# Kernel tuning notes

Hardware: AMD Instinct MI355X
Metric: run time of the kernel (lower is better)

Reference implementation:

```python
import jax, jax.numpy as jnp
import numpy as np

EPS = 1e-15
PROJ_EPS = 1e-5
N_NODES = 100000

def _norm(x):
    return jnp.maximum(jnp.sqrt(jnp.sum(x * x, axis=-1, keepdims=True)), EPS)

def _tanh(x):
    return jnp.tanh(jnp.clip(x, -15.0, 15.0))

def _atanh(x):
    return jnp.arctanh(jnp.clip(x, -1.0 + 1e-7, 1.0 - 1e-7))

def log_map_zero(y):
    n = _norm(y)
    return (_atanh(n) / n) * y

def exp_map_zero(v):
    n = _norm(v)
    return (_tanh(n) / n) * v

def hyperbolic_projection(x):
    # clip norm to 1 - PROJ_EPS (stay inside the Poincare ball)
    n = _norm(x)
    scale = jnp.minimum(jnp.float32(1.0), (1.0 - PROJ_EPS) / n)
    return x * scale

def mobius_addition(x, y):
    x2 = jnp.sum(x * x, axis=-1, keepdims=True)
    y2 = jnp.sum(y * y, axis=-1, keepdims=True)
    xy = jnp.sum(x * y, axis=-1, keepdims=True)
    num = (1.0 + 2.0 * xy + y2) * x + (1.0 - x2) * y
    den = 1.0 + 2.0 * xy + x2 * y2
    return num / jnp.maximum(den, EPS)

def setup_inputs() -> dict:
    key = jax.random.key(0)
    k0, k1, k2, k3, k4, k5 = jax.random.split(key, 6)
    N, E, D_IN, D_OUT = N_NODES, 640000, 128, 128
    # entity embeddings: points inside the Poincare ball
    x = jax.random.normal(k0, (N, D_IN), dtype=jnp.float32) * 0.01
    x = hyperbolic_projection(x)
    # xavier-uniform weight
    a = np.sqrt(6.0 / (D_IN + D_OUT)).astype(np.float32)
    W = jax.random.uniform(k1, (D_IN, D_OUT), minval=-a, maxval=a, dtype=jnp.float32)
    bias = jax.random.normal(k2, (1, D_OUT), dtype=jnp.float32) * 0.01
    adj_row = jax.random.randint(k3, (E,), 0, N, dtype=jnp.int32)
    adj_col = jax.random.randint(k4, (E,), 0, N, dtype=jnp.int32)
    adj_val = jax.random.uniform(k5, (E,), dtype=jnp.float32) * 0.125
    return {"ents_embed_input": x, "W_ent": W, "bias_vec": bias,
            "adj_val": adj_val, "adj_row": adj_row, "adj_col": adj_col}

def reference(ents_embed_input, W_ent, bias_vec, adj_val, adj_row, adj_col):
    # log map to tangent space at origin, then dense linear map
    tangent = log_map_zero(ents_embed_input)                 # [N, D_in]
    mapped = tangent @ W_ent                                 # [N, D_out]
    # sparse adjacency aggregation: out[i] = sum_e val[e] * mapped[col[e]], row[e] == i
    msgs = adj_val[:, None] * mapped[adj_col]                # [E, D_out]
    agg = jax.ops.segment_sum(msgs, adj_row, num_segments=N_NODES)
    h = hyperbolic_projection(exp_map_zero(agg))
    # mobius bias addition
    b = hyperbolic_projection(exp_map_zero(bias_vec))
    out = hyperbolic_projection(mobius_addition(h, b))
    return out
```

## Files before the change

kernel.cpp:

```cpp
#include <hip/hip_runtime.h>
#include <hip/hip_bf16.h>

#define D 128
#define FEPS 1e-15f
#define PROJ_EPS 1e-5f

typedef __attribute__((ext_vector_type(8))) short short8v;
typedef __attribute__((ext_vector_type(4))) float f32x4;

__device__ __forceinline__ unsigned pack_bf16x2(float lo, float hi) {
    __hip_bfloat16 h0 = __float2bfloat16(lo);
    __hip_bfloat16 h1 = __float2bfloat16(hi);
    unsigned u0 = *reinterpret_cast<unsigned short*>(&h0);
    unsigned u1 = *reinterpret_cast<unsigned short*>(&h1);
    return u0 | (u1 << 16);
}

__device__ __forceinline__ float bf_lo(unsigned u) { return __uint_as_float(u << 16); }
__device__ __forceinline__ float bf_hi(unsigned u) { return __uint_as_float(u & 0xffff0000u); }

__device__ __forceinline__ float fast_tanh_clamped(float n) {
    float nc = fminf(n, 15.f);
    float e2 = __expf(2.f * nc);
    return 1.f - __fdividef(2.f, e2 + 1.f);
}

__global__ __launch_bounds__(512) void k_hist8(const int* __restrict__ rowi,
                                               int* __restrict__ cnt8,
                                               int E, int Nn, int Eper) {
    int e = blockIdx.x * 512 + threadIdx.x;
    if (e < E) {
        int g = e / Eper;
        atomicAdd(&cnt8[(size_t)g * Nn + rowi[e]], 1);
    }
}

__global__ __launch_bounds__(256) void k_scan1(const int* __restrict__ cnt,
                                               int* __restrict__ ex,
                                               int* __restrict__ bsum, int Ntot) {
    __shared__ int ts[256];
    int t = threadIdx.x, b = blockIdx.x;
    int base = b * 1024 + t * 4;
    int v0 = (base + 0 < Ntot) ? cnt[base + 0] : 0;
    int v1 = (base + 1 < Ntot) ? cnt[base + 1] : 0;
    int v2 = (base + 2 < Ntot) ? cnt[base + 2] : 0;
    int v3 = (base + 3 < Ntot) ? cnt[base + 3] : 0;
    int s = v0 + v1 + v2 + v3;
    ts[t] = s;
    __syncthreads();
    for (int off = 1; off < 256; off <<= 1) {
        int add = (t >= off) ? ts[t - off] : 0;
        __syncthreads();
        ts[t] += add;
        __syncthreads();
    }
    int excl = ts[t] - s;
    if (t == 255) bsum[b] = ts[t];
    if (base + 0 < Ntot) ex[base + 0] = excl;
    if (base + 1 < Ntot) ex[base + 1] = excl + v0;
    if (base + 2 < Ntot) ex[base + 2] = excl + v0 + v1;
    if (base + 3 < Ntot) ex[base + 3] = excl + v0 + v1 + v2;
}

__global__ __launch_bounds__(1024) void k_scan2(const int* __restrict__ bsum,
                                                int* __restrict__ bsumx, int nb) {
    __shared__ int ts[1024];
    int t = threadIdx.x;
    int v = (t < nb) ? bsum[t] : 0;
    ts[t] = v;
    __syncthreads();
    for (int off = 1; off < 1024; off <<= 1) {
        int add = (t >= off) ? ts[t - off] : 0;
        __syncthreads();
        ts[t] += add;
        __syncthreads();
    }
    bsumx[t] = ts[t] - v;
}

__global__ __launch_bounds__(256) void k_scan3(int* __restrict__ base8,
                                               const int* __restrict__ bsumx,
                                               int* __restrict__ cursor8,
                                               int Ntot, int E) {
    int i = blockIdx.x * 256 + threadIdx.x;
    if (i < Ntot) {
        int v = base8[i] + bsumx[i >> 10];
        base8[i] = v;
        cursor8[i] = v;
    }
    if (i == 0) base8[Ntot] = E;
}

__global__ __launch_bounds__(512) void k_gemm_scatter(
    const float* __restrict__ x, const float* __restrict__ W,
    __hip_bfloat16* __restrict__ mapped, int Nn, int NT, int GBg,
    const int* __restrict__ rowi, const int* __restrict__ coli,
    const float* __restrict__ val, int* __restrict__ cursor8,
    int2* __restrict__ sedge, int E)
{
    __shared__ uint4 lsW4[2048];
    __shared__ uint4 lsC4[2048];

    const int tid = threadIdx.x;

    if (blockIdx.x >= GBg) {
        const int j = blockIdx.x - GBg;
        const int g = j & 7;
        const int ib = j >> 3;
        const int Echunk = (E + 127) >> 7;
        const int chunk = g * 16 + ib;
        int e0 = chunk * Echunk;
        int e1 = min(e0 + Echunk, E);
        int* cur = cursor8 + (size_t)g * Nn;
        for (int e = e0 + tid; e < e1; e += 512) {
            int r = rowi[e];
            int cv = coli[e];
            float vv = val[e];
            int p = atomicAdd(&cur[r], 1);
            sedge[p] = make_int2(cv, __float_as_int(vv));
        }
        return;
    }

    const int w = tid >> 6, l = tid & 63;
    const int q = l & 15, khi = l >> 4;

#pragma unroll
    for (int it = 0; it < 4; ++it) {
        int i = it * 512 + tid;
        int col = i & 127, kg = i >> 7;
        unsigned p0 = pack_bf16x2(W[(kg * 8 + 0) * D + col], W[(kg * 8 + 1) * D + col]);
        unsigned p1 = pack_bf16x2(W[(kg * 8 + 2) * D + col], W[(kg * 8 + 3) * D + col]);
        unsigned p2 = pack_bf16x2(W[(kg * 8 + 4) * D + col], W[(kg * 8 + 5) * D + col]);
        unsigned p3 = pack_bf16x2(W[(kg * 8 + 6) * D + col], W[(kg * 8 + 7) * D + col]);
        lsW4[col * 16 + (kg ^ (col & 15))] = make_uint4(p0, p1, p2, p3);
    }
    __syncthreads();

    const short8v* lsB = (const short8v*)lsW4;
    unsigned* lsc = (unsigned*)lsC4;
    const int cbase = w * 1024;

#pragma unroll 1
    for (int tt = blockIdx.x; tt < NT; tt += GBg) {
        const int rowbase = tt * 128;
        const int row = rowbase + w * 16 + q;
        const bool rv = row < Nn;
        const float* xr = x + (size_t)row * D;
        float4 xa[8];
        float nn = 0.f;
#pragma unroll
        for (int ks = 0; ks < 4; ++ks) {
            float4 p0 = make_float4(0.f, 0.f, 0.f, 0.f), p1 = p0;
            if (rv) {
                p0 = *reinterpret_cast<const float4*>(xr + ks * 32 + khi * 8);
                p1 = *reinterpret_cast<const float4*>(xr + ks * 32 + khi * 8 + 4);
            }
            xa[2 * ks] = p0; xa[2 * ks + 1] = p1;
            nn += p0.x * p0.x + p0.y * p0.y + p0.z * p0.z + p0.w * p0.w
                + p1.x * p1.x + p1.y * p1.y + p1.z * p1.z + p1.w * p1.w;
        }
        nn += __shfl_xor(nn, 16, 64);
        nn += __shfl_xor(nn, 32, 64);
        float n = fmaxf(sqrtf(nn), FEPS);
        float c = fminf(n, 1.f - 1e-7f);
        float s = __fdividef(0.5f * __logf(__fdividef(1.f + c, 1.f - c)), n);

        union { unsigned u[4]; short8v v; } af[4];
#pragma unroll
        for (int ks = 0; ks < 4; ++ks) {
            float4 p0 = xa[2 * ks], p1 = xa[2 * ks + 1];
            af[ks].u[0] = pack_bf16x2(s * p0.x, s * p0.y);
            af[ks].u[1] = pack_bf16x2(s * p0.z, s * p0.w);
            af[ks].u[2] = pack_bf16x2(s * p1.x, s * p1.y);
            af[ks].u[3] = pack_bf16x2(s * p1.z, s * p1.w);
        }

        f32x4 acc[8];
#pragma unroll
        for (int t = 0; t < 8; ++t) acc[t] = (f32x4){0.f, 0.f, 0.f, 0.f};

#pragma unroll
        for (int ks = 0; ks < 4; ++ks) {
#pragma unroll
            for (int t = 0; t < 8; ++t) {
                short8v b = lsB[(t * 16 + q) * 16 + ((ks * 4 + khi) ^ q)];
                acc[t] = __builtin_amdgcn_mfma_f32_16x16x32_bf16(af[ks].v, b, acc[t], 0, 0, 0);
            }
        }

#pragma unroll
        for (int t = 0; t < 8; ++t) {
#pragma unroll
            for (int r = 0; r < 4; ++r) {
                float self = acc[t][r];
                float other = __shfl_xor(self, 1, 64);
                unsigned pw = (q & 1) ? pack_bf16x2(other, self) : pack_bf16x2(self, other);
                int rl = khi * 4 + r;
                int cp = t * 8 + (q >> 1);
                lsc[cbase + rl * 64 + (cp ^ (khi << 3))] = pw;
            }
        }
#pragma unroll
        for (int i4 = 0; i4 < 4; ++i4) {
            int rl = i4 * 4 + (l >> 4);
            int ro = rowbase + w * 16 + rl;
            int cp4 = (l & 15) * 4;
            uint4 vv = lsC4[(cbase + rl * 64 + (cp4 ^ (i4 << 3))) >> 2];
            if (ro < Nn)
                *reinterpret_cast<uint4*>(mapped + (size_t)ro * D + (l & 15) * 8) = vv;
        }
    }
}

__device__ __forceinline__ void accum8(float* acc, uint4 u, float v) {
    acc[0] += v * bf_lo(u.x); acc[1] += v * bf_hi(u.x);
    acc[2] += v * bf_lo(u.y); acc[3] += v * bf_hi(u.y);
    acc[4] += v * bf_lo(u.z); acc[5] += v * bf_hi(u.z);
    acc[6] += v * bf_lo(u.w); acc[7] += v * bf_hi(u.w);
}

__global__ __launch_bounds__(256) void k_aggfin(
    const uint4* __restrict__ mapped4, const int2* __restrict__ sedge,
    const int* __restrict__ base8, const float* __restrict__ bias,
    float* __restrict__ out, int Nn)
{
    const int tid = threadIdx.x;
    const int w = tid >> 6, l = tid & 63;
    const int g = l >> 4, q = l & 15;
    const int row = blockIdx.x * 16 + w * 4 + g;

    float4 rb0 = *reinterpret_cast<const float4*>(bias + q * 8);
    float4 rb1 = *reinterpret_cast<const float4*>(bias + q * 8 + 4);
    float bn2 = rb0.x * rb0.x + rb0.y * rb0.y + rb0.z * rb0.z + rb0.w * rb0.w
              + rb1.x * rb1.x + rb1.y * rb1.y + rb1.z * rb1.z + rb1.w * rb1.w;
#pragma unroll
    for (int o = 8; o > 0; o >>= 1) bn2 += __shfl_xor(bn2, o, 64);
    float bn = fmaxf(sqrtf(bn2), FEPS);
    float bt = fast_tanh_clamped(bn);
    float bs = __fdividef(bt, bn);
    float ben2 = bs * bs * bn2;
    float bpn = fmaxf(sqrtf(ben2), FEPS);
    float bps = fminf(1.f, __fdividef(1.f - PROJ_EPS, bpn));
    float bsc = bs * bps;
    float y2 = bps * bps * ben2;
    float bj[8] = { rb0.x * bsc, rb0.y * bsc, rb0.z * bsc, rb0.w * bsc,
                    rb1.x * bsc, rb1.y * bsc, rb1.z * bsc, rb1.w * bsc };

    if (row >= Nn) return;

    int hdr = base8[(size_t)(q & 7) * Nn + row + (q >> 3)];
    const int gl = l & 48;
    int b[8], en_[8];
#pragma unroll
    for (int s2 = 0; s2 < 8; ++s2) {
        b[s2]   = __shfl(hdr, gl + s2, 64);
        en_[s2] = __shfl(hdr, gl + 8 + s2, 64);
    }

    float acc[8] = {0.f, 0.f, 0.f, 0.f, 0.f, 0.f, 0.f, 0.f};
    while (true) {
        int2 d[4]; bool h[4];
#pragma unroll
        for (int s = 0; s < 4; ++s) {
            int p = -1;
            if (b[s] < en_[s])            { p = b[s]; b[s] += 1; }
            else if (b[s + 4] < en_[s + 4]) { p = b[s + 4]; b[s + 4] += 1; }
            h[s] = (p >= 0);
            if (h[s]) d[s] = sedge[p];
        }
        uint4 u[4];
#pragma unroll
        for (int s = 0; s < 4; ++s)
            if (h[s]) u[s] = mapped4[(size_t)d[s].x * 16 + q];
#pragma unroll
        for (int s = 0; s < 4; ++s)
            if (h[s]) accum8(acc, u[s], __int_as_float(d[s].y));
        bool any = false;
#pragma unroll
        for (int s = 0; s < 8; ++s) any = any || (b[s] < en_[s]);
        if (!any) break;
    }

    float n2 = 0.f, ab = 0.f;
#pragma unroll
    for (int j = 0; j < 8; ++j) { n2 += acc[j] * acc[j]; ab += acc[j] * bj[j]; }
#pragma unroll
    for (int o = 8; o > 0; o >>= 1) {
        n2 += __shfl_xor(n2, o, 64);
        ab += __shfl_xor(ab, o, 64);
    }

    float n = fmaxf(sqrtf(n2), FEPS);
    float t = fast_tanh_clamped(n);
    float s = __fdividef(t, n);
    float en2 = s * s * n2;
    float pn = fmaxf(sqrtf(en2), FEPS);
    float ps = fminf(1.f, __fdividef(1.f - PROJ_EPS, pn));
    float hs = s * ps;
    float x2 = ps * ps * en2;

    float xy = hs * ab;
    float cA = 1.f + 2.f * xy + y2;
    float cB = 1.f - x2;
    float den = fmaxf(1.f + 2.f * xy + x2 * y2, FEPS);
    float inv = __fdividef(1.f, den);
    float zn2 = inv * inv * (cA * cA * x2 + 2.f * cA * cB * xy + cB * cB * y2);
    float zn = fmaxf(sqrtf(zn2), FEPS);
    float zs = fminf(1.f, __fdividef(1.f - PROJ_EPS, zn));
    float f = inv * zs;
    float chs = cA * hs * f, cBf = cB * f;

    float4 o0 = make_float4(chs * acc[0] + cBf * bj[0], chs * acc[1] + cBf * bj[1],
                            chs * acc[2] + cBf * bj[2], chs * acc[3] + cBf * bj[3]);
    float4 o1 = make_float4(chs * acc[4] + cBf * bj[4], chs * acc[5] + cBf * bj[5],
                            chs * acc[6] + cBf * bj[6], chs * acc[7] + cBf * bj[7]);
    *reinterpret_cast<float4*>(out + (size_t)row * D + q * 8) = o0;
    *reinterpret_cast<float4*>(out + (size_t)row * D + q * 8 + 4) = o1;
}

extern "C" void kernel_launch(void* const* d_in, const int* in_sizes, int n_in,
                              void* d_out, int out_size, void* d_ws, size_t ws_size,
                              hipStream_t stream) {
    const float* x    = (const float*)d_in[0];
    const float* W    = (const float*)d_in[1];
    const float* bias = (const float*)d_in[2];
    const float* val  = (const float*)d_in[3];
    const int*   rowi = (const int*)d_in[4];
    const int*   coli = (const int*)d_in[5];
    const int N = in_sizes[0] / D;
    const int E = in_sizes[3];
    const int N8 = 8 * N;

    char* ws = (char*)d_ws;
    size_t off = 0;
    int* cnt8 = (int*)(ws + off);      off += (size_t)N8 * 4;
    int* base8 = (int*)(ws + off);     off += ((size_t)N8 + 1) * 4;
    off = (off + 63) & ~(size_t)63;
    int* bsum = (int*)(ws + off);      off += 1024 * 4;
    int* bsumx = (int*)(ws + off);     off += 1024 * 4;
    int* cursor8 = (int*)(ws + off);   off += (size_t)N8 * 4;
    off = (off + 63) & ~(size_t)63;
    int2* sedge = (int2*)(ws + off);   off += (size_t)E * 8;
    __hip_bfloat16* mapped = (__hip_bfloat16*)(ws + off);
    float* out = (float*)d_out;

    const int Echunk = (E + 127) >> 7;
    const int Eper = 16 * Echunk;

    hipMemsetAsync(cnt8, 0, (size_t)N8 * sizeof(int), stream);
    k_hist8<<<(E + 511) / 512, 512, 0, stream>>>(rowi, cnt8, E, N, Eper);

    int nb = (N8 + 1023) / 1024;
    k_scan1<<<nb, 256, 0, stream>>>(cnt8, base8, bsum, N8);
    k_scan2<<<1, 1024, 0, stream>>>(bsum, bsumx, nb);
    k_scan3<<<(N8 + 255) / 256, 256, 0, stream>>>(base8, bsumx, cursor8, N8, E);

    const int NT  = (N + 127) / 128;
    const int GBg = 384;
    k_gemm_scatter<<<GBg + 128, 512, 0, stream>>>(x, W, mapped, N, NT, GBg,
                                                  rowi, coli, val, cursor8, sedge, E);

    k_aggfin<<<(N + 15) / 16, 256, 0, stream>>>((const uint4*)mapped,
                                                (const int2*)sedge, base8,
                                                bias, out, N);
}
```

Baseline: 149.7 us.

## Replace per-row CSR sort with 120-row bucket binning and LDS atomic aggregation

Drops the 8-way per-row histogram and three-pass scan. Edges are instead binned into buckets of 120 destination rows, so only about 834 bucket counters need a single-block scan. The scatter blocks now do a block-local counting sort in shared memory before writing coalesced records. Aggregation runs one block per bucket and accumulates into a shared-memory float tile with LDS atomics. This cuts scan and global-atomic overhead but adds shared-memory atomic contention, wider 16-byte edge records, and makes the float summation order nondeterministic.

```diff
diff --git a/kernel.cpp b/kernel.cpp
--- a/kernel.cpp
+++ b/kernel.cpp
@@ -4,6 +4,9 @@
 #define D 128
 #define FEPS 1e-15f
 #define PROJ_EPS 1e-5f
+#define BROWS 120
+#define BSTRIDE 132
+#define SC 3072
 
 typedef __attribute__((ext_vector_type(8))) short short8v;
 typedef __attribute__((ext_vector_type(4))) float f32x4;
@@ -25,48 +28,18 @@
     return 1.f - __fdividef(2.f, e2 + 1.f);
 }
 
-__global__ __launch_bounds__(512) void k_hist8(const int* __restrict__ rowi,
-                                               int* __restrict__ cnt8,
-                                               int E, int Nn, int Eper) {
+__global__ __launch_bounds__(512) void k_bhist(const int* __restrict__ rowi,
+                                               int* __restrict__ bcntP, int E) {
     int e = blockIdx.x * 512 + threadIdx.x;
-    if (e < E) {
-        int g = e / Eper;
-        atomicAdd(&cnt8[(size_t)g * Nn + rowi[e]], 1);
-    }
-}
-
-__global__ __launch_bounds__(256) void k_scan1(const int* __restrict__ cnt,
-                                               int* __restrict__ ex,
-                                               int* __restrict__ bsum, int Ntot) {
-    __shared__ int ts[256];
-    int t = threadIdx.x, b = blockIdx.x;
-    int base = b * 1024 + t * 4;
-    int v0 = (base + 0 < Ntot) ? cnt[base + 0] : 0;
-    int v1 = (base + 1 < Ntot) ? cnt[base + 1] : 0;
-    int v2 = (base + 2 < Ntot) ? cnt[base + 2] : 0;
-    int v3 = (base + 3 < Ntot) ? cnt[base + 3] : 0;
-    int s = v0 + v1 + v2 + v3;
-    ts[t] = s;
-    __syncthreads();
-    for (int off = 1; off < 256; off <<= 1) {
-        int add = (t >= off) ? ts[t - off] : 0;
-        __syncthreads();
-        ts[t] += add;
-        __syncthreads();
-    }
-    int excl = ts[t] - s;
-    if (t == 255) bsum[b] = ts[t];
-    if (base + 0 < Ntot) ex[base + 0] = excl;
-    if (base + 1 < Ntot) ex[base + 1] = excl + v0;
-    if (base + 2 < Ntot) ex[base + 2] = excl + v0 + v1;
-    if (base + 3 < Ntot) ex[base + 3] = excl + v0 + v1 + v2;
-}
-
-__global__ __launch_bounds__(1024) void k_scan2(const int* __restrict__ bsum,
-                                                int* __restrict__ bsumx, int nb) {
+    if (e < E) atomicAdd(&bcntP[(rowi[e] / BROWS) * 16], 1);
+}
+
+__global__ __launch_bounds__(1024) void k_bscan(const int* __restrict__ bcntP,
+                                                int* __restrict__ bbase,
+                                                int* __restrict__ bcursor, int NB) {
     __shared__ int ts[1024];
     int t = threadIdx.x;
-    int v = (t < nb) ? bsum[t] : 0;
+    int v = (t < NB) ? bcntP[t * 16] : 0;
     ts[t] = v;
     __syncthreads();
     for (int off = 1; off < 1024; off <<= 1) {
@@ -75,53 +48,99 @@
         ts[t] += add;
         __syncthreads();
     }
-    bsumx[t] = ts[t] - v;
-}
-
-__global__ __launch_bounds__(256) void k_scan3(int* __restrict__ base8,
-                                               const int* __restrict__ bsumx,
-                                               int* __restrict__ cursor8,
-                                               int Ntot, int E) {
-    int i = blockIdx.x * 256 + threadIdx.x;
-    if (i < Ntot) {
-        int v = base8[i] + bsumx[i >> 10];
-        base8[i] = v;
-        cursor8[i] = v;
-    }
-    if (i == 0) base8[Ntot] = E;
-}
-
-__global__ __launch_bounds__(512) void k_gemm_scatter(
+    int ex = ts[t] - v;
+    if (t < NB) { bbase[t] = ex; bcursor[t] = ex; }
+    if (t == NB - 1) bbase[NB] = ex + v;
+}
+
+__global__ __launch_bounds__(512) void k_gemm_bin(
     const float* __restrict__ x, const float* __restrict__ W,
-    __hip_bfloat16* __restrict__ mapped, int Nn, int NT, int GBg,
+    __hip_bfloat16* __restrict__ mapped, int Nn, int NT, int GBg, int SBb,
     const int* __restrict__ rowi, const int* __restrict__ coli,
-    const float* __restrict__ val, int* __restrict__ cursor8,
-    int2* __restrict__ sedge, int E)
+    const float* __restrict__ val, int* __restrict__ bcursor,
+    int4* __restrict__ brec, int E, int NB)
 {
-    __shared__ uint4 lsW4[2048];
-    __shared__ uint4 lsC4[2048];
+    __shared__ uint4 ls4[4096];
 
     const int tid = threadIdx.x;
 
     if (blockIdx.x >= GBg) {
+        char* base = (char*)ls4;
+        int4* srec  = (int4*)base;
+        int* lhist  = (int*)(base + 49152);
+        int* lstart = (int*)(base + 53248);
+        int* gb     = (int*)(base + 57344);
+        int* scr    = (int*)(base + 60704);
+
         const int j = blockIdx.x - GBg;
-        const int g = j & 7;
-        const int ib = j >> 3;
-        const int Echunk = (E + 127) >> 7;
-        const int chunk = g * 16 + ib;
-        int e0 = chunk * Echunk;
-        int e1 = min(e0 + Echunk, E);
-        int* cur = cursor8 + (size_t)g * Nn;
-        for (int e = e0 + tid; e < e1; e += 512) {
-            int r = rowi[e];
-            int cv = coli[e];
-            float vv = val[e];
-            int p = atomicAdd(&cur[r], 1);
-            sedge[p] = make_int2(cv, __float_as_int(vv));
+        const int NC = (E + SC - 1) / SC;
+        for (int ci = j; ci < NC; ci += SBb) {
+            const int e0 = ci * SC;
+            const int cnt = min(SC, E - e0);
+
+            for (int b = tid; b < 1024; b += 512) lhist[b] = 0;
+            __syncthreads();
+
+            int rr[6], cc[6], vi[6], bb[6];
+#pragma unroll
+            for (int k = 0; k < 6; ++k) {
+                int idx = k * 512 + tid;
+                if (idx < cnt) {
+                    int e = e0 + idx;
+                    rr[k] = rowi[e]; cc[k] = coli[e];
+                    vi[k] = __float_as_int(val[e]);
+                    bb[k] = rr[k] / BROWS;
+                    atomicAdd(&lhist[bb[k]], 1);
+                }
+            }
+            __syncthreads();
+
+            {
+                int a0 = lhist[2 * tid], a1 = lhist[2 * tid + 1];
+                int ps = a0 + a1;
+                scr[tid] = ps;
+                __syncthreads();
+                for (int off = 1; off < 512; off <<= 1) {
+                    int add = (tid >= off) ? scr[tid - off] : 0;
+                    __syncthreads();
+                    scr[tid] += add;
+                    __syncthreads();
+                }
+                int ex = scr[tid] - ps;
+                lstart[2 * tid] = ex;
+                lstart[2 * tid + 1] = ex + a0;
+            }
+            __syncthreads();
+            for (int b = tid; b < 840; b += 512) scr[b] = lstart[b];
+            __syncthreads();
+
+#pragma unroll
+            for (int k = 0; k < 6; ++k) {
+                int idx = k * 512 + tid;
+                if (idx < cnt) {
+                    int slot = atomicAdd(&scr[bb[k]], 1);
+                    srec[slot] = make_int4(rr[k], cc[k], vi[k], bb[k]);
+                }
+            }
+            __syncthreads();
+
+            for (int b = tid; b < NB; b += 512) {
+                int cb = lhist[b];
+                gb[b] = cb ? atomicAdd(&bcursor[b], cb) : 0;
+            }
+            __syncthreads();
+
+            for (int i = tid; i < cnt; i += 512) {
+                int4 rec = srec[i];
+                brec[gb[rec.w] + (i - lstart[rec.w])] = rec;
+            }
+            __syncthreads();
         }
         return;
     }
 
+    uint4* lsW4 = ls4;
+    uint4* lsC4 = ls4 + 2048;
     const int w = tid >> 6, l = tid & 63;
     const int q = l & 15, khi = l >> 4;
 
@@ -179,7 +198,6 @@
         f32x4 acc[8];
 #pragma unroll
         for (int t = 0; t < 8; ++t) acc[t] = (f32x4){0.f, 0.f, 0.f, 0.f};
-
 #pragma unroll
         for (int ks = 0; ks < 4; ++ks) {
 #pragma unroll
@@ -213,25 +231,23 @@
     }
 }
 
-__device__ __forceinline__ void accum8(float* acc, uint4 u, float v) {
-    acc[0] += v * bf_lo(u.x); acc[1] += v * bf_hi(u.x);
-    acc[2] += v * bf_lo(u.y); acc[3] += v * bf_hi(u.y);
-    acc[4] += v * bf_lo(u.z); acc[5] += v * bf_hi(u.z);
-    acc[6] += v * bf_lo(u.w); acc[7] += v * bf_hi(u.w);
-}
-
-__global__ __launch_bounds__(256) void k_aggfin(
-    const uint4* __restrict__ mapped4, const int2* __restrict__ sedge,
-    const int* __restrict__ base8, const float* __restrict__ bias,
+__global__ __launch_bounds__(512) void k_aggfin_lds(
+    const uint2* __restrict__ mapped2, const int4* __restrict__ brec,
+    const int* __restrict__ bbase, const float* __restrict__ bias,
     float* __restrict__ out, int Nn)
 {
+    __shared__ float facc[BROWS][BSTRIDE];
+
     const int tid = threadIdx.x;
-    const int w = tid >> 6, l = tid & 63;
-    const int g = l >> 4, q = l & 15;
-    const int row = blockIdx.x * 16 + w * 4 + g;
-
-    float4 rb0 = *reinterpret_cast<const float4*>(bias + q * 8);
-    float4 rb1 = *reinterpret_cast<const float4*>(bias + q * 8 + 4);
+    const int l = tid & 63;
+    const int q = l & 15;
+
+    float4* fz = (float4*)&facc[0][0];
+    for (int i = tid; i < (BROWS * BSTRIDE) / 4; i += 512)
+        fz[i] = make_float4(0.f, 0.f, 0.f, 0.f);
+
+    float4 rb0 = *reinterpret_cast<const float4*>(bias + 4 * q);
+    float4 rb1 = *reinterpret_cast<const float4*>(bias + 64 + 4 * q);
     float bn2 = rb0.x * rb0.x + rb0.y * rb0.y + rb0.z * rb0.z + rb0.w * rb0.w
               + rb1.x * rb1.x + rb1.y * rb1.y + rb1.z * rb1.z + rb1.w * rb1.w;
 #pragma unroll
@@ -247,76 +263,75 @@
     float bj[8] = { rb0.x * bsc, rb0.y * bsc, rb0.z * bsc, rb0.w * bsc,
                     rb1.x * bsc, rb1.y * bsc, rb1.z * bsc, rb1.w * bsc };
 
-    if (row >= Nn) return;
-
-    int hdr = base8[(size_t)(q & 7) * Nn + row + (q >> 3)];
-    const int gl = l & 48;
-    int b[8], en_[8];
-#pragma unroll
-    for (int s2 = 0; s2 < 8; ++s2) {
-        b[s2]   = __shfl(hdr, gl + s2, 64);
-        en_[s2] = __shfl(hdr, gl + 8 + s2, 64);
-    }
-
-    float acc[8] = {0.f, 0.f, 0.f, 0.f, 0.f, 0.f, 0.f, 0.f};
-    while (true) {
-        int2 d[4]; bool h[4];
-#pragma unroll
-        for (int s = 0; s < 4; ++s) {
-            int p = -1;
-            if (b[s] < en_[s])            { p = b[s]; b[s] += 1; }
-            else if (b[s + 4] < en_[s + 4]) { p = b[s + 4]; b[s + 4] += 1; }
-            h[s] = (p >= 0);
-            if (h[s]) d[s] = sedge[p];
-        }
-        uint4 u[4];
-#pragma unroll
-        for (int s = 0; s < 4; ++s)
-            if (h[s]) u[s] = mapped4[(size_t)d[s].x * 16 + q];
-#pragma unroll
-        for (int s = 0; s < 4; ++s)
-            if (h[s]) accum8(acc, u[s], __int_as_float(d[s].y));
-        bool any = false;
-#pragma unroll
-        for (int s = 0; s < 8; ++s) any = any || (b[s] < en_[s]);
-        if (!any) break;
-    }
-
-    float n2 = 0.f, ab = 0.f;
-#pragma unroll
-    for (int j = 0; j < 8; ++j) { n2 += acc[j] * acc[j]; ab += acc[j] * bj[j]; }
-#pragma unroll
-    for (int o = 8; o > 0; o >>= 1) {
-        n2 += __shfl_xor(n2, o, 64);
-        ab += __shfl_xor(ab, o, 64);
-    }
-
-    float n = fmaxf(sqrtf(n2), FEPS);
-    float t = fast_tanh_clamped(n);
-    float s = __fdividef(t, n);
-    float en2 = s * s * n2;
-    float pn = fmaxf(sqrtf(en2), FEPS);
-    float ps = fminf(1.f, __fdividef(1.f - PROJ_EPS, pn));
-    float hs = s * ps;
-    float x2 = ps * ps * en2;
-
-    float xy = hs * ab;
-    float cA = 1.f + 2.f * xy + y2;
-    float cB = 1.f - x2;
-    float den = fmaxf(1.f + 2.f * xy + x2 * y2, FEPS);
-    float inv = __fdividef(1.f, den);
-    float zn2 = inv * inv * (cA * cA * x2 + 2.f * cA * cB * xy + cB * cB * y2);
-    float zn = fmaxf(sqrtf(zn2), FEPS);
-    float zs = fminf(1.f, __fdividef(1.f - PROJ_EPS, zn));
-    float f = inv * zs;
-    float chs = cA * hs * f, cBf = cB * f;
-
-    float4 o0 = make_float4(chs * acc[0] + cBf * bj[0], chs * acc[1] + cBf * bj[1],
-                            chs * acc[2] + cBf * bj[2], chs * acc[3] + cBf * bj[3]);
-    float4 o1 = make_float4(chs * acc[4] + cBf * bj[4], chs * acc[5] + cBf * bj[5],
-                            chs * acc[6] + cBf * bj[6], chs * acc[7] + cBf * bj[7]);
-    *reinterpret_cast<float4*>(out + (size_t)row * D + q * 8) = o0;
-    *reinterpret_cast<float4*>(out + (size_t)row * D + q * 8 + 4) = o1;
+    __syncthreads();
+
+    const int bkt = blockIdx.x;
+    const int beg = bbase[bkt], end = bbase[bkt + 1];
+    const int grp = tid >> 4;
+
+    for (int e = beg + grp; e < end; e += 32) {
+        int4 rec = brec[e];
+        float v = __int_as_float(rec.z);
+        int rl = rec.x - bkt * BROWS;
+        uint2 m0 = mapped2[(size_t)rec.y * 32 + q];
+        uint2 m1 = mapped2[(size_t)rec.y * 32 + 16 + q];
+        atomicAdd(&facc[rl][4 * q + 0], v * bf_lo(m0.x));
+        atomicAdd(&facc[rl][4 * q + 1], v * bf_hi(m0.x));
+        atomicAdd(&facc[rl][4 * q + 2], v * bf_lo(m0.y));
+        atomicAdd(&facc[rl][4 * q + 3], v * bf_hi(m0.y));
+        atomicAdd(&facc[rl][64 + 4 * q + 0], v * bf_lo(m1.x));
+        atomicAdd(&facc[rl][64 + 4 * q + 1], v * bf_hi(m1.x));
+        atomicAdd(&facc[rl][64 + 4 * q + 2], v * bf_lo(m1.y));
+        atomicAdd(&facc[rl][64 + 4 * q + 3], v * bf_hi(m1.y));
+    }
+    __syncthreads();
+
+    const int w = tid >> 6, g = l >> 4;
+#pragma unroll
+    for (int r4 = 0; r4 < 4; ++r4) {
+        int rl = w * 16 + r4 * 4 + g;
+        int row = bkt * BROWS + rl;
+        if (rl >= BROWS || row >= Nn) continue;
+        float4 f0 = *(float4*)&facc[rl][4 * q];
+        float4 f1 = *(float4*)&facc[rl][64 + 4 * q];
+        float a[8] = { f0.x, f0.y, f0.z, f0.w, f1.x, f1.y, f1.z, f1.w };
+
+        float n2 = 0.f, ab = 0.f;
+#pragma unroll
+        for (int jj = 0; jj < 8; ++jj) { n2 += a[jj] * a[jj]; ab += a[jj] * bj[jj]; }
+#pragma unroll
+        for (int o = 8; o > 0; o >>= 1) {
+            n2 += __shfl_xor(n2, o, 64);
+            ab += __shfl_xor(ab, o, 64);
+        }
+
+        float n = fmaxf(sqrtf(n2), FEPS);
+        float t = fast_tanh_clamped(n);
+        float s = __fdividef(t, n);
+        float en2 = s * s * n2;
+        float pn = fmaxf(sqrtf(en2), FEPS);
+        float ps = fminf(1.f, __fdividef(1.f - PROJ_EPS, pn));
+        float hs = s * ps;
+        float x2 = ps * ps * en2;
+
+        float xy = hs * ab;
+        float cA = 1.f + 2.f * xy + y2;
+        float cB = 1.f - x2;
+        float den = fmaxf(1.f + 2.f * xy + x2 * y2, FEPS);
+        float inv = __fdividef(1.f, den);
+        float zn2 = inv * inv * (cA * cA * x2 + 2.f * cA * cB * xy + cB * cB * y2);
+        float zn = fmaxf(sqrtf(zn2), FEPS);
+        float zs = fminf(1.f, __fdividef(1.f - PROJ_EPS, zn));
+        float f = inv * zs;
+        float chs = cA * hs * f, cBf = cB * f;
+
+        float4 o0 = make_float4(chs * a[0] + cBf * bj[0], chs * a[1] + cBf * bj[1],
+                                chs * a[2] + cBf * bj[2], chs * a[3] + cBf * bj[3]);
+        float4 o1 = make_float4(chs * a[4] + cBf * bj[4], chs * a[5] + cBf * bj[5],
+                                chs * a[6] + cBf * bj[6], chs * a[7] + cBf * bj[7]);
+        *reinterpret_cast<float4*>(out + (size_t)row * D + 4 * q) = o0;
+        *reinterpret_cast<float4*>(out + (size_t)row * D + 64 + 4 * q) = o1;
+    }
 }
 
 extern "C" void kernel_launch(void* const* d_in, const int* in_sizes, int n_in,
@@ -330,38 +345,28 @@
     const int*   coli = (const int*)d_in[5];
     const int N = in_sizes[0] / D;
     const int E = in_sizes[3];
-    const int N8 = 8 * N;
+    const int NB = (N + BROWS - 1) / BROWS;
 
     char* ws = (char*)d_ws;
     size_t off = 0;
-    int* cnt8 = (int*)(ws + off);      off += (size_t)N8 * 4;
-    int* base8 = (int*)(ws + off);     off += ((size_t)N8 + 1) * 4;
-    off = (off + 63) & ~(size_t)63;
-    int* bsum = (int*)(ws + off);      off += 1024 * 4;
-    int* bsumx = (int*)(ws + off);     off += 1024 * 4;
-    int* cursor8 = (int*)(ws + off);   off += (size_t)N8 * 4;
-    off = (off + 63) & ~(size_t)63;
-    int2* sedge = (int2*)(ws + off);   off += (size_t)E * 8;
+    int* bcntP  = (int*)(ws + off);  off += (size_t)NB * 64;
+    int* bbase  = (int*)(ws + off);  off += ((size_t)NB + 1) * 4;
+    int* bcursor= (int*)(ws + off);  off += (size_t)NB * 4;
+    off = (off + 15) & ~(size_t)15;
+    int4* brec  = (int4*)(ws + off); off += (size_t)E * 16;
     __hip_bfloat16* mapped = (__hip_bfloat16*)(ws + off);
     float* out = (float*)d_out;
 
-    const int Echunk = (E + 127) >> 7;
-    const int Eper = 16 * Echunk;
-
-    hipMemsetAsync(cnt8, 0, (size_t)N8 * sizeof(int), stream);
-    k_hist8<<<(E + 511) / 512, 512, 0, stream>>>(rowi, cnt8, E, N, Eper);
-
-    int nb = (N8 + 1023) / 1024;
-    k_scan1<<<nb, 256, 0, stream>>>(cnt8, base8, bsum, N8);
-    k_scan2<<<1, 1024, 0, stream>>>(bsum, bsumx, nb);
-    k_scan3<<<(N8 + 255) / 256, 256, 0, stream>>>(base8, bsumx, cursor8, N8, E);
+    hipMemsetAsync(bcntP, 0, (size_t)NB * 64, stream);
+    k_bhist<<<(E + 511) / 512, 512, 0, stream>>>(rowi, bcntP, E);
+    k_bscan<<<1, 1024, 0, stream>>>(bcntP, bbase, bcursor, NB);
 
     const int NT  = (N + 127) / 128;
     const int GBg = 384;
-    k_gemm_scatter<<<GBg + 128, 512, 0, stream>>>(x, W, mapped, N, NT, GBg,
-                                                  rowi, coli, val, cursor8, sedge, E);
-
-    k_aggfin<<<(N + 15) / 16, 256, 0, stream>>>((const uint4*)mapped,
-                                                (const int2*)sedge, base8,
-                                                bias, out, N);
-}
+    const int SBb = 128;
+    k_gemm_bin<<<GBg + SBb, 512, 0, stream>>>(x, W, mapped, N, NT, GBg, SBb,
+                                              rowi, coli, val, bcursor, brec, E, NB);
+
+    k_aggfin_lds<<<NB, 512, 0, stream>>>((const uint2*)mapped, brec, bbase,
+                                         bias, out, N);
+}
```

After: 580.0 us. 3.88x slower.
